# Kernel tuning notes

Measured on AMD Instinct MI355X. Metric: run time of the kernel, lower is better.

The kernel has to match this reference:

```python
import jax, jax.numpy as jnp
import numpy as np


def conv2d(x, w, b, pad=1):
    y = jax.lax.conv_general_dilated(x, w, (1, 1), [(pad, pad), (pad, pad)],
                                     dimension_numbers=('NCHW', 'OIHW', 'NCHW'))
    return y + b[None, :, None, None]


def deform_conv2d(x, offsets, w, b, groups=8, pad=1):
    # torchvision-style deformable conv: offsets [B, 2*G*K, H, W] laid out as
    # (g, k, (dy, dx)); input channels split into G offset groups; zero padding
    # outside the image for bilinear sampling.
    B, C, H, W = x.shape
    kh, kw = w.shape[2], w.shape[3]
    K = kh * kw
    cpg = C // groups
    off = offsets.reshape(B, groups, K, 2, H, W)
    dy, dx = off[:, :, :, 0], off[:, :, :, 1]  # [B,G,K,H,W]
    ky, kx = jnp.meshgrid(jnp.arange(kh), jnp.arange(kw), indexing='ij')
    ky = ky.reshape(K).astype(x.dtype)
    kx = kx.reshape(K).astype(x.dtype)
    ygrid = jnp.arange(H, dtype=x.dtype)
    xgrid = jnp.arange(W, dtype=x.dtype)
    # absolute sampling positions [B,G,K,H,W]
    py = ygrid[None, None, None, :, None] + (ky - pad)[None, None, :, None, None] + dy
    px = xgrid[None, None, None, None, :] + (kx - pad)[None, None, :, None, None] + dx
    y0 = jnp.floor(py)
    x0 = jnp.floor(px)
    wy = py - y0  # frac weights [B,G,K,H,W]
    wx = px - x0
    y0i = y0.astype(jnp.int32)
    x0i = x0.astype(jnp.int32)
    xg = x.reshape(B, groups, cpg, H * W)

    def gather(yc, xc):
        valid = ((yc >= 0) & (yc < H) & (xc >= 0) & (xc < W)).astype(x.dtype)
        idx = jnp.clip(yc, 0, H - 1) * W + jnp.clip(xc, 0, W - 1)
        idx = jnp.broadcast_to(idx.reshape(B, groups, 1, K * H * W),
                               (B, groups, cpg, K * H * W))
        v = jnp.take_along_axis(xg, idx, axis=3).reshape(B, groups, cpg, K, H, W)
        return v * valid[:, :, None]

    v00 = gather(y0i, x0i)
    v01 = gather(y0i, x0i + 1)
    v10 = gather(y0i + 1, x0i)
    v11 = gather(y0i + 1, x0i + 1)
    wy_ = wy[:, :, None]  # [B,G,1,K,H,W]
    wx_ = wx[:, :, None]
    sampled = (v00 * (1 - wy_) * (1 - wx_) + v01 * (1 - wy_) * wx_
               + v10 * wy_ * (1 - wx_) + v11 * wy_ * wx_)
    sampled = sampled.reshape(B, C, K, H, W)
    out = jnp.einsum('bckhw,ock->bohw', sampled, w.reshape(w.shape[0], C, K))
    return out + b[None, :, None, None]


def dab(feat, aux_in, aux_w, aux_b, fw1, fb1, fw2, fb2, se_w1, se_b1, se_w2, se_b2):
    # Adaptive fusion block: project aux (128->64), concat, conv-relu-conv body,
    # SE channel attention (reduction=2), residual add onto feat.
    aux = jax.nn.relu(conv2d(aux_in, aux_w, aux_b))
    x = jnp.concatenate([feat, aux], axis=1)  # [B,128,H,W]
    x = jax.nn.relu(conv2d(x, fw1, fb1))      # 128->64
    x = conv2d(x, fw2, fb2)                   # 64->64
    g = jnp.mean(x, axis=(2, 3))              # [B,64]
    a = jax.nn.sigmoid(jax.nn.relu(g @ se_w1.T + se_b1) @ se_w2.T + se_b2)
    return feat + x * a[:, :, None, None]


def setup_inputs() -> dict:
    key = jax.random.key(0)
    ks = jax.random.split(key, 16)
    B, H, W = 4, 192, 192

    def p(k, shape, s=0.05):
        return jax.random.normal(k, shape, jnp.float32) * s

    return {
        'mv': jax.random.normal(ks[0], (B, 128, H, W), jnp.float32),
        'ref_feature': jax.random.normal(ks[1], (B, 64, H, W), jnp.float32),
        'head_w': p(ks[2], (144, 128, 3, 3)), 'head_b': jnp.zeros((144,), jnp.float32),
        'dcn_w': p(ks[3], (64, 64, 3, 3)), 'dcn_b': jnp.zeros((64,), jnp.float32),
        'c1w1': p(ks[4], (128, 64, 3, 3)), 'c1b1': jnp.zeros((128,), jnp.float32),
        'c1w2': p(ks[5], (128, 128, 3, 3)), 'c1b2': jnp.zeros((128,), jnp.float32),
        'aux_w': p(ks[6], (64, 128, 3, 3)), 'aux_b': jnp.zeros((64,), jnp.float32),
        'fw1': p(ks[7], (64, 128, 3, 3)), 'fb1': jnp.zeros((64,), jnp.float32),
        'fw2': p(ks[8], (64, 64, 3, 3)), 'fb2': jnp.zeros((64,), jnp.float32),
        'se_w1': p(ks[9], (32, 64)), 'se_b1': jnp.zeros((32,), jnp.float32),
        'se_w2': p(ks[10], (64, 32)), 'se_b2': jnp.zeros((64,), jnp.float32),
    }


def reference(mv, ref_feature, head_w, head_b, dcn_w, dcn_b, c1w1, c1b1, c1w2, c1b2,
              aux_w, aux_b, fw1, fb1, fw2, fb2, se_w1, se_b1, se_w2, se_b2):
    offsets = conv2d(mv, head_w, head_b)                       # [B,144,H,W]
    def_feat = jax.nn.relu(deform_conv2d(ref_feature, offsets, dcn_w, dcn_b))
    aux_in = jax.nn.relu(conv2d(jax.nn.relu(conv2d(ref_feature, c1w1, c1b1)),
                                c1w2, c1b2))                   # convs1: 64->128->128
    return dab(def_feat, aux_in, aux_w, aux_b, fw1, fb1, fw2, fb2,
               se_w1, se_b1, se_w2, se_b2)
```

## Files before the change

kernel.cpp:

```cpp
#include <hip/hip_runtime.h>
#include <math.h>

#define HH 192
#define WW 192
#define HWSZ (HH*WW)
#define BB 4

typedef __attribute__((ext_vector_type(8))) short bf16x8;
typedef __attribute__((ext_vector_type(4))) float f32x4;

__device__ __forceinline__ unsigned short f2bf(float f) {
    unsigned int u = __float_as_uint(f);
    u = (u + 0x7FFFu + ((u >> 16) & 1u)) >> 16;
    return (unsigned short)u;
}
__device__ __forceinline__ float bf2f(unsigned short s) {
    return __uint_as_float(((unsigned int)s) << 16);
}

__global__ void prep_all(
    const float* __restrict__ head_w, const float* __restrict__ c1w1,
    const float* __restrict__ c1w2,   const float* __restrict__ aux_w,
    const float* __restrict__ fw1,    const float* __restrict__ fw2,
    const float* __restrict__ dcn_w,
    unsigned short* __restrict__ wb_head, unsigned short* __restrict__ wb_c1w1,
    unsigned short* __restrict__ wb_c1w2, unsigned short* __restrict__ wb_aux,
    unsigned short* __restrict__ wb_fw1,  unsigned short* __restrict__ wb_fw2,
    unsigned short* __restrict__ wdefb2)
{
    int idx = blockIdx.x * 256 + threadIdx.x;
    const float* w; unsigned short* wb; int cout, cin;
    if (idx < 165888)                 { w = head_w; wb = wb_head; cout = 144; cin = 128; }
    else if ((idx -= 165888) < 73728) { w = c1w1;   wb = wb_c1w1; cout = 128; cin = 64;  }
    else if ((idx -= 73728) < 147456) { w = c1w2;   wb = wb_c1w2; cout = 128; cin = 128; }
    else if ((idx -= 147456) < 73728) { w = aux_w;  wb = wb_aux;  cout = 64;  cin = 128; }
    else if ((idx -= 73728) < 73728)  { w = fw1;    wb = wb_fw1;  cout = 64;  cin = 128; }
    else if ((idx -= 73728) < 36864)  { w = fw2;    wb = wb_fw2;  cout = 64;  cin = 64;  }
    else if ((idx -= 36864) < 36864) {
        int o = idx / 576, rem = idx % 576;
        int c = rem / 9, k = rem - c * 9;
        int K = k * 64 + c;
        wdefb2[((size_t)((K >> 5) * 64 + o)) * 32 + (K & 31)] = f2bf(dcn_w[idx]);
        return;
    } else return;
    int o = idx / (cin * 9);
    int rem = idx - o * cin * 9;
    int c = rem / 9;
    int t = rem - c * 9;
    int nch = cin >> 5;
    wb[((t * nch + (c >> 5)) * cout + o) * 32 + (c & 31)] = f2bf(w[idx]);
}

__global__ __launch_bounds__(256) void transpose_all(
    const float* __restrict__ mv, const float* __restrict__ ref,
    unsigned short* __restrict__ mvb, unsigned short* __restrict__ refb)
{
    __shared__ float tile[32][68];
    const int tid = threadIdx.x;
    int bz = blockIdx.z;
    const float* in; unsigned short* outb;
    if (bz < 16) { in = mv;  outb = mvb;  }
    else         { in = ref; outb = refb; bz -= 16; }
    const int y = blockIdx.y;
    const int x0 = blockIdx.x * 64;
#pragma unroll
    for (int it = 0; it < 2; ++it) {
        int u = tid + it * 256;
        int c = u >> 4, q = u & 15;
        float4 v = *(const float4*)(in + (((size_t)bz * 32 + c) * HH + y) * WW + x0 + q * 4);
        *(float4*)&tile[c][q * 4] = v;
    }
    __syncthreads();
    const int pxl = tid >> 2, c8 = tid & 3;
    bf16x8 ov;
#pragma unroll
    for (int j = 0; j < 8; ++j) ov[j] = (short)f2bf(tile[c8 * 8 + j][pxl]);
    *(bf16x8*)(outb + (((size_t)bz * HH + y) * WW + x0 + pxl) * 32 + c8 * 8) = ov;
}

template<int CIN, int COUT_TILE, bool RELU, int EPI>
__global__ __launch_bounds__(256, 3) void conv3x3_v7(
    const unsigned short* __restrict__ in, const unsigned short* __restrict__ wb,
    const float* __restrict__ bias, void* __restrict__ outp,
    int cTot, int ocBase, int nOc, int coutFull, int nPerXcd)
{
    constexpr int NCH = CIN / 32;
    constexpr int NOC = COUT_TILE / 16;
    __shared__ __align__(16) unsigned short sx[6 * 72 * 32];

    const int tid = threadIdx.x;
    const int d = blockIdx.x;
    const int w = (d & 7) * nPerXcd + (d >> 3);
    const int ocT = (w % nOc) * COUT_TILE;
    int t = w / nOc;
    const int x0 = (t % 3) * 64; t /= 3;
    const int y0 = (t % 48) * 4;
    const int b  = t / 48;
    const int wv = tid >> 6, lane = tid & 63;
    const int l15 = lane & 15, kg = lane >> 4;

    f32x4 acc[NOC][4];
#pragma unroll
    for (int oc = 0; oc < NOC; ++oc)
#pragma unroll
        for (int s = 0; s < 4; ++s) acc[oc][s] = (f32x4){0.f, 0.f, 0.f, 0.f};

    for (int ch = 0; ch < NCH; ++ch) {
#pragma unroll
        for (int it = 0; it < 7; ++it) {
            int u = tid + it * 256;
            if (u < 1728) {
                int r = u / 288;
                int rem = u - r * 288;
                int px = rem >> 2, c8 = rem & 3;
                int yin = y0 - 1 + r;
                int gx  = x0 - 4 + px;
                bf16x8 v = {0,0,0,0,0,0,0,0};
                if (yin >= 0 && yin < HH && gx >= 0 && gx < WW)
                    v = *(const bf16x8*)(in + (((size_t)(b * NCH + ch) * HH + yin) * WW + gx) * 32 + c8 * 8);
                *(bf16x8*)&sx[(r * 72 + px) * 32 + ((c8 ^ ((px >> 1) & 3)) << 3)] = v;
            }
        }
        __syncthreads();
#pragma unroll
        for (int ky = 0; ky < 3; ++ky) {
#pragma unroll
            for (int kx = 0; kx < 3; ++kx) {
                const int r = wv + ky;
                bf16x8 bf[4];
#pragma unroll
                for (int s = 0; s < 4; ++s) {
                    int p = s * 16 + l15 + kx + 3;
                    bf[s] = *(const bf16x8*)&sx[(r * 72 + p) * 32 + ((kg ^ ((p >> 1) & 3)) << 3)];
                }
                const unsigned short* wp = wb
                    + ((size_t)(((ky * 3 + kx) * NCH + ch) * coutFull) + ocT + l15) * 32 + kg * 8;
#pragma unroll
                for (int oc = 0; oc < NOC; ++oc) {
                    bf16x8 a = *(const bf16x8*)(wp + oc * 16 * 32);
#pragma unroll
                    for (int s = 0; s < 4; ++s)
                        acc[oc][s] = __builtin_amdgcn_mfma_f32_16x16x32_bf16(a, bf[s], acc[oc][s], 0, 0, 0);
                }
            }
        }
        __syncthreads();
    }
    const int y = y0 + wv;
    if (EPI == 1) {
        float* out = (float*)outp;
#pragma unroll
        for (int oc = 0; oc < NOC; ++oc)
#pragma unroll
            for (int s = 0; s < 4; ++s) {
                int xo = x0 + s * 16 + l15;
#pragma unroll
                for (int j = 0; j < 4; ++j) {
                    int oL = ocT + oc * 16 + kg * 4 + j;
                    float rv = acc[oc][s][j] + bias[oL];
                    if (RELU) rv = fmaxf(rv, 0.f);
                    out[((size_t)(b * cTot + ocBase + oL) * HH + y) * WW + xo] = rv;
                }
            }
    } else if (EPI == 2) {
        unsigned short* out = (unsigned short*)outp;
#pragma unroll
        for (int oc = 0; oc < NOC; ++oc)
#pragma unroll
            for (int s = 0; s < 4; ++s) {
                int xo = x0 + s * 16 + l15;
#pragma unroll
                for (int j = 0; j < 4; ++j) {
                    int oL = ocT + oc * 16 + kg * 4 + j;
                    float rv = acc[oc][s][j] + bias[oL];
                    if (RELU) rv = fmaxf(rv, 0.f);
                    out[((size_t)(b * cTot + ocBase + oL) * HH + y) * WW + xo] = f2bf(rv);
                }
            }
    } else {
        unsigned short* out = (unsigned short*)outp;
#pragma unroll
        for (int oc = 0; oc < NOC; ++oc) {
            int oL = ocT + oc * 16 + kg * 4;
            int o0 = ocBase + oL;
#pragma unroll
            for (int s = 0; s < 4; ++s) {
                int xo = x0 + s * 16 + l15;
                ushort4 u;
                float r0 = acc[oc][s][0] + bias[oL + 0];
                float r1 = acc[oc][s][1] + bias[oL + 1];
                float r2 = acc[oc][s][2] + bias[oL + 2];
                float r3 = acc[oc][s][3] + bias[oL + 3];
                if (RELU) { r0 = fmaxf(r0,0.f); r1 = fmaxf(r1,0.f); r2 = fmaxf(r2,0.f); r3 = fmaxf(r3,0.f); }
                u.x = f2bf(r0); u.y = f2bf(r1); u.z = f2bf(r2); u.w = f2bf(r3);
                *(ushort4*)(out + ((((size_t)(b * cTot + (o0 >> 5)) * HH + y) * WW + xo) * 32) + (o0 & 31)) = u;
            }
        }
    }
}

__global__ __launch_bounds__(512, 4) void deform_v6(
    const unsigned short* __restrict__ xb, const unsigned short* __restrict__ offb,
    const unsigned short* __restrict__ wdefb2, const float* __restrict__ bias,
    unsigned short* __restrict__ cat)
{
    __shared__ __align__(16) unsigned short smp[64 * 584];
    const int tid = threadIdx.x;
    const int b = blockIdx.z;
    int flat = blockIdx.x;
    int nf = (flat & 7) * 72 + (flat >> 3);
    const int pixbase = nf * 64;

    const int px = tid & 63, g = tid >> 6;
    const int pix = pixbase + px;
    const int y = pix / WW, x = pix - y * WW;

    const char* xgb = (const char*)(xb + ((size_t)(b * 2 + (g >> 2)) * HWSZ) * 32 + (g & 3) * 8);
    const unsigned short* ob = offb + ((size_t)(b * 144 + g * 18)) * HWSZ + pix;

    float dyv[9], dxv[9];
#pragma unroll
    for (int k = 0; k < 9; ++k) {
        dyv[k] = bf2f(ob[(size_t)(2 * k) * HWSZ]);
        dxv[k] = bf2f(ob[(size_t)(2 * k + 1) * HWSZ]);
    }

    auto calc = [&](int k, int vo[4], float w4[4]) {
        float pyf = (float)(y + k / 3 - 1) + dyv[k];
        float pxf = (float)(x + k % 3 - 1) + dxv[k];
        float fy = floorf(pyf), fx = floorf(pxf);
        float wy = pyf - fy, wx = pxf - fx;
        int iy = (int)fy, ix = (int)fx;
        float w00 = (1.f - wy) * (1.f - wx), w01 = (1.f - wy) * wx;
        float w10 = wy * (1.f - wx),         w11 = wy * wx;
        bool y0v = (iy >= 0) && (iy < HH);
        bool y1v = (iy + 1 >= 0) && (iy + 1 < HH);
        bool x0v = (ix >= 0) && (ix < WW);
        bool x1v = (ix + 1 >= 0) && (ix + 1 < WW);
        if (!(y0v && x0v)) w00 = 0.f;
        if (!(y0v && x1v)) w01 = 0.f;
        if (!(y1v && x0v)) w10 = 0.f;
        if (!(y1v && x1v)) w11 = 0.f;
        int cy0 = min(max(iy, 0), HH - 1), cy1 = min(max(iy + 1, 0), HH - 1);
        int cx0 = min(max(ix, 0), WW - 1), cx1 = min(max(ix + 1, 0), WW - 1);
        vo[0] = (cy0 * WW + cx0) * 64;
        vo[1] = (cy0 * WW + cx1) * 64;
        vo[2] = (cy1 * WW + cx0) * 64;
        vo[3] = (cy1 * WW + cx1) * 64;
        w4[0] = w00; w4[1] = w01; w4[2] = w10; w4[3] = w11;
    };

    float wr[3][4];
    bf16x8 pf[2][4];
    {
        int vo[4]; calc(0, vo, wr[0]);
#pragma unroll
        for (int j = 0; j < 4; ++j) pf[0][j] = *(const bf16x8*)(xgb + vo[j]);
    }
    {
        int vo[4]; calc(1, vo, wr[1]);
#pragma unroll
        for (int j = 0; j < 4; ++j) pf[1][j] = *(const bf16x8*)(xgb + vo[j]);
    }
    unsigned short* so = smp + px * 584 + g * 8;
#pragma unroll
    for (int k = 0; k < 9; ++k) {
        bf16x8 nx0, nx1, nx2, nx3;
        if (k + 2 < 9) {
            int vo[4]; calc(k + 2, vo, wr[(k + 2) % 3]);
            nx0 = *(const bf16x8*)(xgb + vo[0]);
            nx1 = *(const bf16x8*)(xgb + vo[1]);
            nx2 = *(const bf16x8*)(xgb + vo[2]);
            nx3 = *(const bf16x8*)(xgb + vo[3]);
        }
        __builtin_amdgcn_sched_barrier(0);
        bf16x8 ov;
#pragma unroll
        for (int cc = 0; cc < 8; ++cc) {
            float s = bf2f((unsigned short)pf[k & 1][0][cc]) * wr[k % 3][0]
                    + bf2f((unsigned short)pf[k & 1][1][cc]) * wr[k % 3][1]
                    + bf2f((unsigned short)pf[k & 1][2][cc]) * wr[k % 3][2]
                    + bf2f((unsigned short)pf[k & 1][3][cc]) * wr[k % 3][3];
            ov[cc] = (short)f2bf(s);
        }
        *(bf16x8*)(so + k * 64) = ov;
        if (k + 2 < 9) { pf[k & 1][0] = nx0; pf[k & 1][1] = nx1; pf[k & 1][2] = nx2; pf[k & 1][3] = nx3; }
    }
    __syncthreads();
    const int wv = tid >> 6;
    const int lane = tid & 63, l15 = lane & 15, kg = lane >> 4;
    const int oc = wv >> 1, sp = (wv & 1) * 2;
    f32x4 acc0 = (f32x4){0.f, 0.f, 0.f, 0.f};
    f32x4 acc1 = (f32x4){0.f, 0.f, 0.f, 0.f};
    const unsigned short* arow = wdefb2 + ((size_t)(oc * 16 + l15)) * 32 + kg * 8;
#pragma unroll
    for (int ch = 0; ch < 18; ++ch) {
        bf16x8 b0 = *(const bf16x8*)&smp[(sp * 16 + l15) * 584 + ch * 32 + kg * 8];
        bf16x8 b1 = *(const bf16x8*)&smp[((sp + 1) * 16 + l15) * 584 + ch * 32 + kg * 8];
        bf16x8 a = *(const bf16x8*)(arow + (size_t)ch * 64 * 32);
        acc0 = __builtin_amdgcn_mfma_f32_16x16x32_bf16(a, b0, acc0, 0, 0, 0);
        acc1 = __builtin_amdgcn_mfma_f32_16x16x32_bf16(a, b1, acc1, 0, 0, 0);
    }
    const int o0 = oc * 16 + kg * 4;
#pragma unroll
    for (int s = 0; s < 2; ++s) {
        const f32x4& av = s ? acc1 : acc0;
        int pxo = pixbase + (sp + s) * 16 + l15;
        int yo = pxo / WW, xo = pxo - yo * WW;
        ushort4 u;
        u.x = f2bf(fmaxf(av[0] + bias[o0 + 0], 0.f));
        u.y = f2bf(fmaxf(av[1] + bias[o0 + 1], 0.f));
        u.z = f2bf(fmaxf(av[2] + bias[o0 + 2], 0.f));
        u.w = f2bf(fmaxf(av[3] + bias[o0 + 3], 0.f));
        *(ushort4*)(cat + ((((size_t)(b * 4 + (o0 >> 5)) * HH + yo) * WW + xo) * 32) + (o0 & 31)) = u;
    }
}

__global__ __launch_bounds__(256) void pool_kernel(const float* __restrict__ x, float* __restrict__ gout)
{
    int bc = blockIdx.x;
    const float* p = x + (size_t)bc * HWSZ;
    int tid = threadIdx.x;
    float s = 0.f;
    for (int i = tid * 4; i < HWSZ; i += 256 * 4) {
        float4 v = *reinterpret_cast<const float4*>(p + i);
        s += v.x + v.y + v.z + v.w;
    }
#pragma unroll
    for (int o = 32; o > 0; o >>= 1) s += __shfl_down(s, o, 64);
    __shared__ float red[4];
    if ((tid & 63) == 0) red[tid >> 6] = s;
    __syncthreads();
    if (tid == 0) gout[bc] = (red[0] + red[1] + red[2] + red[3]) * (1.f / (float)HWSZ);
}

__global__ __launch_bounds__(256) void se_kernel(
    const float* __restrict__ g, const float* __restrict__ w1, const float* __restrict__ b1,
    const float* __restrict__ w2, const float* __restrict__ b2, float* __restrict__ a)
{
    __shared__ float sg[BB * 64];
    __shared__ float sh[BB * 32];
    int tid = threadIdx.x;
    sg[tid] = g[tid];
    __syncthreads();
    if (tid < BB * 32) {
        int b = tid / 32, h = tid % 32;
        float s = b1[h];
        for (int c = 0; c < 64; ++c) s += sg[b * 64 + c] * w1[h * 64 + c];
        sh[b * 32 + h] = fmaxf(s, 0.f);
    }
    __syncthreads();
    {
        int b = tid / 64, o = tid % 64;
        float s = b2[o];
        for (int h = 0; h < 32; ++h) s += sh[b * 32 + h] * w2[o * 32 + h];
        a[tid] = 1.f / (1.f + expf(-s));
    }
}

__global__ __launch_bounds__(256) void final_v2(
    float* __restrict__ out, const unsigned short* __restrict__ catb, const float* __restrict__ a)
{
    const int VPC = HWSZ / 4;
    int v = blockIdx.x * 256 + threadIdx.x;
    int bc = v / VPC, within = v - bc * VPC;
    int b = bc >> 6, c = bc & 63;
    float av = a[bc];
    int pix = within * 4;
    int y = pix / WW, x = pix - y * WW;
    const unsigned short* dbase = catb
        + (((size_t)(b * 4 + (c >> 5)) * HH + y) * WW + x) * 32 + (c & 31);
    float4 xo = reinterpret_cast<float4*>(out)[v];
    float4 r;
    r.x = bf2f(dbase[0])  + xo.x * av;
    r.y = bf2f(dbase[32]) + xo.y * av;
    r.z = bf2f(dbase[64]) + xo.z * av;
    r.w = bf2f(dbase[96]) + xo.w * av;
    reinterpret_cast<float4*>(out)[v] = r;
}

extern "C" void kernel_launch(void* const* d_in, const int* in_sizes, int n_in,
                              void* d_out, int out_size, void* d_ws, size_t ws_size,
                              hipStream_t stream) {
    const float* mv     = (const float*)d_in[0];
    const float* ref    = (const float*)d_in[1];
    const float* head_w = (const float*)d_in[2];
    const float* head_b = (const float*)d_in[3];
    const float* dcn_w  = (const float*)d_in[4];
    const float* dcn_b  = (const float*)d_in[5];
    const float* c1w1   = (const float*)d_in[6];
    const float* c1b1   = (const float*)d_in[7];
    const float* c1w2   = (const float*)d_in[8];
    const float* c1b2   = (const float*)d_in[9];
    const float* aux_w  = (const float*)d_in[10];
    const float* aux_b  = (const float*)d_in[11];
    const float* fw1    = (const float*)d_in[12];
    const float* fb1    = (const float*)d_in[13];
    const float* fw2    = (const float*)d_in[14];
    const float* fb2    = (const float*)d_in[15];
    const float* se_w1  = (const float*)d_in[16];
    const float* se_b1  = (const float*)d_in[17];
    const float* se_w2  = (const float*)d_in[18];
    const float* se_b2  = (const float*)d_in[19];
    float* out = (float*)d_out;

    float* ws = (float*)d_ws;
    unsigned short* offb     = (unsigned short*)ws;
    unsigned short* mvb      = (unsigned short*)(ws + 21233664);
    unsigned short* refb     = (unsigned short*)(ws + 30670848);
    unsigned short* catb     = (unsigned short*)(ws + 35389440);
    unsigned short* r2b      = (unsigned short*)(ws + 44826624);
    unsigned short* wdefb2   = (unsigned short*)(ws + 54263808);
    unsigned short* wbb      = (unsigned short*)(ws + 54282240);
    float* gbuf              = ws + 54567936;
    float* abuf              = gbuf + 256;
    unsigned short* t1b      = (unsigned short*)ws;

    unsigned short* wb_head = wbb;
    unsigned short* wb_c1w1 = wb_head + 165888;
    unsigned short* wb_c1w2 = wb_c1w1 + 73728;
    unsigned short* wb_aux  = wb_c1w2 + 147456;
    unsigned short* wb_fw1  = wb_aux  + 73728;
    unsigned short* wb_fw2  = wb_fw1  + 73728;

    prep_all<<<2376, 256, 0, stream>>>(head_w, c1w1, c1w2, aux_w, fw1, fw2, dcn_w,
                                       wb_head, wb_c1w1, wb_c1w2, wb_aux, wb_fw1, wb_fw2, wdefb2);
    transpose_all<<<dim3(3, 192, 24), 256, 0, stream>>>(mv, ref, mvb, refb);

    conv3x3_v7<128, 48, false, 2><<<1728, 256, 0, stream>>>(
        mvb, wb_head, head_b, offb, 144, 0, 3, 144, 216);
    deform_v6<<<dim3(576, 1, BB), 512, 0, stream>>>(refb, offb, wdefb2, dcn_b, catb);
    conv3x3_v7<64, 64, true, 0><<<1152, 256, 0, stream>>>(
        refb, wb_c1w1, c1b1, t1b, 4, 0, 2, 128, 144);
    conv3x3_v7<128, 64, true, 0><<<1152, 256, 0, stream>>>(
        t1b, wb_c1w2, c1b2, r2b, 4, 0, 2, 128, 144);
    conv3x3_v7<128, 32, true, 0><<<1152, 256, 0, stream>>>(
        r2b, wb_aux, aux_b, catb, 4, 64, 2, 64, 144);
    conv3x3_v7<128, 32, true, 0><<<1152, 256, 0, stream>>>(
        catb, wb_fw1, fb1, r2b, 2, 0, 2, 64, 144);
    conv3x3_v7<64, 32, false, 1><<<1152, 256, 0, stream>>>(
        r2b, wb_fw2, fb2, out, 64, 0, 2, 64, 144);
    pool_kernel<<<BB * 64, 256, 0, stream>>>(out, gbuf);
    se_kernel<<<1, 256, 0, stream>>>(gbuf, se_w1, se_b1, se_w2, se_b2, abuf);
    final_v2<<<9216, 256, 0, stream>>>(out, catb, abuf);
}
```

Before: 490.4 us.

## Use zero-padded activation layout and direct global-to-LDS loads in 3x3 convs

Stores all bf16 activation buffers in a spatially padded layout (194x200, with zeroed borders written by a new pad kernel), so the conv tile loader can drop bounds checks. It then issues global_load_lds 16-byte async copies straight into shared memory instead of going through registers. The occupancy hint rises from 3 to 4 blocks per CU. In exchange it adds extra small zeroing launches and a larger workspace, and it relies on the padding borders never being overwritten by the buffers that alias them.

```diff
diff --git a/kernel.cpp b/kernel.cpp
--- a/kernel.cpp
+++ b/kernel.cpp
@@ -5,9 +5,16 @@
 #define WW 192
 #define HWSZ (HH*WW)
 #define BB 4
+#define PH 194
+#define PW 200
+#define CS 1241600
 
 typedef __attribute__((ext_vector_type(8))) short bf16x8;
 typedef __attribute__((ext_vector_type(4))) float f32x4;
+
+#define GLD16(SRC, LDS) __builtin_amdgcn_global_load_lds( \
+    (const __attribute__((address_space(1))) void*)(SRC), \
+    (__attribute__((address_space(3))) void*)(LDS), 16, 0, 0)
 
 __device__ __forceinline__ unsigned short f2bf(float f) {
     unsigned int u = __float_as_uint(f);
@@ -51,6 +58,19 @@
     wb[((t * nch + (c >> 5)) * cout + o) * 32 + (c & 31)] = f2bf(w[idx]);
 }
 
+__global__ void pad_zero_buf(unsigned short* __restrict__ base, int nchunks)
+{
+    int t = blockIdx.x * 256 + threadIdx.x;
+    if (t >= nchunks * 1936) return;
+    int ci = t / 1936, c = t - ci * 1936;
+    int py, pxx;
+    if (c < 400) { py = (c < 200) ? 0 : 193; pxx = c % 200; }
+    else { int c2 = c - 400; py = 1 + (c2 >> 3); int col = c2 & 7; pxx = (col < 4) ? col : 192 + col; }
+    unsigned short* p = base + (size_t)ci * CS + ((size_t)py * PW + pxx) * 32;
+    bf16x8 z = {0,0,0,0,0,0,0,0};
+    *(bf16x8*)(p) = z; *(bf16x8*)(p + 8) = z; *(bf16x8*)(p + 16) = z; *(bf16x8*)(p + 24) = z;
+}
+
 __global__ __launch_bounds__(256) void transpose_all(
     const float* __restrict__ mv, const float* __restrict__ ref,
     unsigned short* __restrict__ mvb, unsigned short* __restrict__ refb)
@@ -75,11 +95,11 @@
     bf16x8 ov;
 #pragma unroll
     for (int j = 0; j < 8; ++j) ov[j] = (short)f2bf(tile[c8 * 8 + j][pxl]);
-    *(bf16x8*)(outb + (((size_t)bz * HH + y) * WW + x0 + pxl) * 32 + c8 * 8) = ov;
+    *(bf16x8*)(outb + (size_t)bz * CS + (((size_t)(y + 1)) * PW + x0 + 4 + pxl) * 32 + c8 * 8) = ov;
 }
 
 template<int CIN, int COUT_TILE, bool RELU, int EPI>
-__global__ __launch_bounds__(256, 3) void conv3x3_v7(
+__global__ __launch_bounds__(256, 4) void conv3x3_v8(
     const unsigned short* __restrict__ in, const unsigned short* __restrict__ wb,
     const float* __restrict__ bias, void* __restrict__ outp,
     int cTot, int ocBase, int nOc, int coutFull, int nPerXcd)
@@ -106,19 +126,17 @@
         for (int s = 0; s < 4; ++s) acc[oc][s] = (f32x4){0.f, 0.f, 0.f, 0.f};
 
     for (int ch = 0; ch < NCH; ++ch) {
+        const unsigned short* chbase = in + (size_t)(b * NCH + ch) * CS;
 #pragma unroll
         for (int it = 0; it < 7; ++it) {
-            int u = tid + it * 256;
-            if (u < 1728) {
+            if (it * 256 + wv * 64 < 1728) {
+                int u = tid + it * 256;
                 int r = u / 288;
                 int rem = u - r * 288;
                 int px = rem >> 2, c8 = rem & 3;
-                int yin = y0 - 1 + r;
-                int gx  = x0 - 4 + px;
-                bf16x8 v = {0,0,0,0,0,0,0,0};
-                if (yin >= 0 && yin < HH && gx >= 0 && gx < WW)
-                    v = *(const bf16x8*)(in + (((size_t)(b * NCH + ch) * HH + yin) * WW + gx) * 32 + c8 * 8);
-                *(bf16x8*)&sx[(r * 72 + px) * 32 + ((c8 ^ ((px >> 1) & 3)) << 3)] = v;
+                const unsigned short* src = chbase
+                    + ((size_t)(y0 + r) * PW + x0 + px) * 32 + ((c8 ^ ((px >> 1) & 3)) << 3);
+                GLD16(src, (char*)sx + it * 4096 + wv * 1024);
             }
         }
         __syncthreads();
@@ -193,13 +211,14 @@
                 float r3 = acc[oc][s][3] + bias[oL + 3];
                 if (RELU) { r0 = fmaxf(r0,0.f); r1 = fmaxf(r1,0.f); r2 = fmaxf(r2,0.f); r3 = fmaxf(r3,0.f); }
                 u.x = f2bf(r0); u.y = f2bf(r1); u.z = f2bf(r2); u.w = f2bf(r3);
-                *(ushort4*)(out + ((((size_t)(b * cTot + (o0 >> 5)) * HH + y) * WW + xo) * 32) + (o0 & 31)) = u;
+                *(ushort4*)(out + (size_t)(b * cTot + (o0 >> 5)) * CS
+                    + (((size_t)(y + 1)) * PW + xo + 4) * 32 + (o0 & 31)) = u;
             }
         }
     }
 }
 
-__global__ __launch_bounds__(512, 4) void deform_v6(
+__global__ __launch_bounds__(512, 4) void deform_v7(
     const unsigned short* __restrict__ xb, const unsigned short* __restrict__ offb,
     const unsigned short* __restrict__ wdefb2, const float* __restrict__ bias,
     unsigned short* __restrict__ cat)
@@ -215,7 +234,7 @@
     const int pix = pixbase + px;
     const int y = pix / WW, x = pix - y * WW;
 
-    const char* xgb = (const char*)(xb + ((size_t)(b * 2 + (g >> 2)) * HWSZ) * 32 + (g & 3) * 8);
+    const char* xgb = (const char*)(xb + (size_t)(b * 2 + (g >> 2)) * CS + (g & 3) * 8);
     const unsigned short* ob = offb + ((size_t)(b * 144 + g * 18)) * HWSZ + pix;
 
     float dyv[9], dxv[9];
@@ -243,10 +262,10 @@
         if (!(y1v && x1v)) w11 = 0.f;
         int cy0 = min(max(iy, 0), HH - 1), cy1 = min(max(iy + 1, 0), HH - 1);
         int cx0 = min(max(ix, 0), WW - 1), cx1 = min(max(ix + 1, 0), WW - 1);
-        vo[0] = (cy0 * WW + cx0) * 64;
-        vo[1] = (cy0 * WW + cx1) * 64;
-        vo[2] = (cy1 * WW + cx0) * 64;
-        vo[3] = (cy1 * WW + cx1) * 64;
+        vo[0] = ((cy0 + 1) * PW + cx0 + 4) * 64;
+        vo[1] = ((cy0 + 1) * PW + cx1 + 4) * 64;
+        vo[2] = ((cy1 + 1) * PW + cx0 + 4) * 64;
+        vo[3] = ((cy1 + 1) * PW + cx1 + 4) * 64;
         w4[0] = w00; w4[1] = w01; w4[2] = w10; w4[3] = w11;
     };
 
@@ -312,7 +331,8 @@
         u.y = f2bf(fmaxf(av[1] + bias[o0 + 1], 0.f));
         u.z = f2bf(fmaxf(av[2] + bias[o0 + 2], 0.f));
         u.w = f2bf(fmaxf(av[3] + bias[o0 + 3], 0.f));
-        *(ushort4*)(cat + ((((size_t)(b * 4 + (o0 >> 5)) * HH + yo) * WW + xo) * 32) + (o0 & 31)) = u;
+        *(ushort4*)(cat + (size_t)(b * 4 + (o0 >> 5)) * CS
+            + (((size_t)(yo + 1)) * PW + xo + 4) * 32 + (o0 & 31)) = u;
     }
 }
 
@@ -358,7 +378,7 @@
     }
 }
 
-__global__ __launch_bounds__(256) void final_v2(
+__global__ __launch_bounds__(256) void final_v3(
     float* __restrict__ out, const unsigned short* __restrict__ catb, const float* __restrict__ a)
 {
     const int VPC = HWSZ / 4;
@@ -368,8 +388,8 @@
     float av = a[bc];
     int pix = within * 4;
     int y = pix / WW, x = pix - y * WW;
-    const unsigned short* dbase = catb
-        + (((size_t)(b * 4 + (c >> 5)) * HH + y) * WW + x) * 32 + (c & 31);
+    const unsigned short* dbase = catb + (size_t)(b * 4 + (c >> 5)) * CS
+        + (((size_t)(y + 1)) * PW + x + 4) * 32 + (c & 31);
     float4 xo = reinterpret_cast<float4*>(out)[v];
     float4 r;
     r.x = bf2f(dbase[0])  + xo.x * av;
@@ -404,17 +424,17 @@
     const float* se_b2  = (const float*)d_in[19];
     float* out = (float*)d_out;
 
-    float* ws = (float*)d_ws;
-    unsigned short* offb     = (unsigned short*)ws;
-    unsigned short* mvb      = (unsigned short*)(ws + 21233664);
-    unsigned short* refb     = (unsigned short*)(ws + 30670848);
-    unsigned short* catb     = (unsigned short*)(ws + 35389440);
-    unsigned short* r2b      = (unsigned short*)(ws + 44826624);
-    unsigned short* wdefb2   = (unsigned short*)(ws + 54263808);
-    unsigned short* wbb      = (unsigned short*)(ws + 54282240);
-    float* gbuf              = ws + 54567936;
-    float* abuf              = gbuf + 256;
-    unsigned short* t1b      = (unsigned short*)ws;
+    unsigned short* wsS = (unsigned short*)d_ws;
+    unsigned short* offb   = wsS;
+    unsigned short* t1b    = wsS;
+    unsigned short* mvb    = wsS + 21233664;
+    unsigned short* refb   = mvb + 16 * (size_t)CS;
+    unsigned short* catb   = refb + 8 * (size_t)CS;
+    unsigned short* r2b    = catb + 16 * (size_t)CS;
+    unsigned short* wdefb2 = r2b + 16 * (size_t)CS;
+    unsigned short* wbb    = wdefb2 + 36864;
+    float* gbuf            = (float*)(wbb + 571392);
+    float* abuf            = gbuf + 256;
 
     unsigned short* wb_head = wbb;
     unsigned short* wb_c1w1 = wb_head + 165888;
@@ -426,21 +446,23 @@
     prep_all<<<2376, 256, 0, stream>>>(head_w, c1w1, c1w2, aux_w, fw1, fw2, dcn_w,
                                        wb_head, wb_c1w1, wb_c1w2, wb_aux, wb_fw1, wb_fw2, wdefb2);
     transpose_all<<<dim3(3, 192, 24), 256, 0, stream>>>(mv, ref, mvb, refb);
-
-    conv3x3_v7<128, 48, false, 2><<<1728, 256, 0, stream>>>(
+    pad_zero_buf<<<424, 256, 0, stream>>>(mvb, 56);
+
+    conv3x3_v8<128, 48, false, 2><<<1728, 256, 0, stream>>>(
         mvb, wb_head, head_b, offb, 144, 0, 3, 144, 216);
-    deform_v6<<<dim3(576, 1, BB), 512, 0, stream>>>(refb, offb, wdefb2, dcn_b, catb);
-    conv3x3_v7<64, 64, true, 0><<<1152, 256, 0, stream>>>(
+    deform_v7<<<dim3(576, 1, BB), 512, 0, stream>>>(refb, offb, wdefb2, dcn_b, catb);
+    pad_zero_buf<<<121, 256, 0, stream>>>(t1b, 16);
+    conv3x3_v8<64, 64, true, 0><<<1152, 256, 0, stream>>>(
         refb, wb_c1w1, c1b1, t1b, 4, 0, 2, 128, 144);
-    conv3x3_v7<128, 64, true, 0><<<1152, 256, 0, stream>>>(
+    conv3x3_v8<128, 64, true, 0><<<1152, 256, 0, stream>>>(
         t1b, wb_c1w2, c1b2, r2b, 4, 0, 2, 128, 144);
-    conv3x3_v7<128, 32, true, 0><<<1152, 256, 0, stream>>>(
+    conv3x3_v8<128, 32, true, 0><<<1152, 256, 0, stream>>>(
         r2b, wb_aux, aux_b, catb, 4, 64, 2, 64, 144);
-    conv3x3_v7<128, 32, true, 0><<<1152, 256, 0, stream>>>(
+    conv3x3_v8<128, 32, true, 0><<<1152, 256, 0, stream>>>(
         catb, wb_fw1, fb1, r2b, 2, 0, 2, 64, 144);
-    conv3x3_v7<64, 32, false, 1><<<1152, 256, 0, stream>>>(
+    conv3x3_v8<64, 32, false, 1><<<1152, 256, 0, stream>>>(
         r2b, wb_fw2, fb2, out, 64, 0, 2, 64, 144);
     pool_kernel<<<BB * 64, 256, 0, stream>>>(out, gbuf);
     se_kernel<<<1, 256, 0, stream>>>(gbuf, se_w1, se_b1, se_w2, se_b2, abuf);
-    final_v2<<<9216, 256, 0, stream>>>(out, catb, abuf);
-}
+    final_v3<<<9216, 256, 0, stream>>>(out, catb, abuf);
+}
```

New measurement: 605.3 us. 1.23x slower.
